# Kernel optimization log

Measured on AMD Instinct MI355X. Metric: run time of the kernel, lower is better.

The kernel has to match this reference:

```python
import jax, jax.numpy as jnp
import numpy as np

TILE = 16


def _tiled_hamilton_transform(tiles, weights):
    """tiles: [B, T, 16, 4]; weights: [T, 16, 16, 4] -> [B, T, 16, 4].

    Equivalent to broadcasting the Hamilton product to [B,T,16,16,4] and
    summing over dim=2, but expressed as 16 small einsum contractions so the
    large intermediate is never materialized.
    """
    a1, b1, c1, d1 = [tiles[..., k] for k in range(4)]      # each [B, T, 16]
    a2, b2, c2, d2 = [weights[..., k] for k in range(4)]    # each [T, 16, 16]

    def ctr(x, w):
        return jnp.einsum('bti,tij->btj', x, w)

    r_a = ctr(a1, a2) - ctr(b1, b2) - ctr(c1, c2) - ctr(d1, d2)
    r_b = ctr(a1, b2) + ctr(b1, a2) + ctr(c1, d2) - ctr(d1, c2)
    r_c = ctr(a1, c2) - ctr(b1, d2) + ctr(c1, a2) + ctr(d1, b2)
    r_d = ctr(a1, d2) + ctr(b1, c2) - ctr(c1, b2) + ctr(d1, a2)
    return jnp.stack([r_a, r_b, r_c, r_d], axis=-1)


def setup_inputs() -> dict:
    key = jax.random.key(0)
    k1, k2, k3 = jax.random.split(key, 3)
    x = jax.random.normal(k1, (65536, 256, 4), dtype=jnp.float32)
    phi_weights = jax.random.normal(k2, (16, 16, 16, 4), dtype=jnp.float32) * 0.02
    psi_weights = jax.random.normal(k3, (16, 16, 16, 4), dtype=jnp.float32) * 0.02
    return {"x": x, "phi_weights": phi_weights, "psi_weights": psi_weights}


def reference(x, phi_weights, psi_weights):
    B, D, _ = x.shape                      # D = manifold_dim = 256
    half_tiles = D // 2 // TILE            # = 8 = num_tiles // 2
    x1, x2 = jnp.split(x, 2, axis=1)       # each [B, 128, 4]
    x1_tiles = x1.reshape(B, half_tiles, TILE, 4)
    x2_tiles = x2.reshape(B, half_tiles, TILE, 4)

    f_out = _tiled_hamilton_transform(x2_tiles, phi_weights[:half_tiles])
    y1_tiles = x1_tiles + f_out
    g_out = _tiled_hamilton_transform(y1_tiles, psi_weights[half_tiles:])
    y2_tiles = x2_tiles + g_out

    y1 = y1_tiles.reshape(B, -1, 4)
    y2 = y2_tiles.reshape(B, -1, 4)
    return jnp.concatenate([y1, y2], axis=1)
```

## Files before the change

kernel.cpp:

```cpp
#include <hip/hip_runtime.h>
#include <hip/hip_bf16.h>


typedef __attribute__((ext_vector_type(8))) short bf16x8;
typedef __attribute__((ext_vector_type(4))) float f32x4;

static __device__ __forceinline__ unsigned short f2bf(float f) {
    unsigned u = __builtin_bit_cast(unsigned, f);
    unsigned r = 0x7FFFu + ((u >> 16) & 1u);
    return (unsigned short)((u + r) >> 16);
}

static __device__ __forceinline__ short hwbf(float f) {
    __hip_bfloat16 h = __float2bfloat16(f);
    return __builtin_bit_cast(short, h);
}

__global__ __launch_bounds__(256)
void prep_kernel(const float4* __restrict__ phi,
                 const float4* __restrict__ psi,
                 unsigned short* __restrict__ mt) {
    __shared__ float Phi[64][64];
    __shared__ float Psi[64][64];
    const int t   = blockIdx.x;
    const int tid = threadIdx.x;
    const int i   = tid >> 4, j = tid & 15;

    {
        float4 w = phi[t * 256 + i * 16 + j];
        float a = w.x, b = w.y, c = w.z, d = w.w;
        Phi[4*i+0][4*j+0]= a; Phi[4*i+0][4*j+1]= b; Phi[4*i+0][4*j+2]= c; Phi[4*i+0][4*j+3]= d;
        Phi[4*i+1][4*j+0]=-b; Phi[4*i+1][4*j+1]= a; Phi[4*i+1][4*j+2]=-d; Phi[4*i+1][4*j+3]= c;
        Phi[4*i+2][4*j+0]=-c; Phi[4*i+2][4*j+1]= d; Phi[4*i+2][4*j+2]= a; Phi[4*i+2][4*j+3]=-b;
        Phi[4*i+3][4*j+0]=-d; Phi[4*i+3][4*j+1]=-c; Phi[4*i+3][4*j+2]= b; Phi[4*i+3][4*j+3]= a;
        float4 v = psi[(8 + t) * 256 + i * 16 + j];
        a = v.x; b = v.y; c = v.z; d = v.w;
        Psi[4*i+0][4*j+0]= a; Psi[4*i+0][4*j+1]= b; Psi[4*i+0][4*j+2]= c; Psi[4*i+0][4*j+3]= d;
        Psi[4*i+1][4*j+0]=-b; Psi[4*i+1][4*j+1]= a; Psi[4*i+1][4*j+2]=-d; Psi[4*i+1][4*j+3]= c;
        Psi[4*i+2][4*j+0]=-c; Psi[4*i+2][4*j+1]= d; Psi[4*i+2][4*j+2]= a; Psi[4*i+2][4*j+3]=-b;
        Psi[4*i+3][4*j+0]=-d; Psi[4*i+3][4*j+1]=-c; Psi[4*i+3][4*j+2]= b; Psi[4*i+3][4*j+3]= a;
    }
    __syncthreads();

    unsigned short* m = mt + t * 16384;
    for (int e = tid; e < 16384; e += 256) {
        const int n = e >> 7, k = e & 127;
        if (n >= 64 && k >= 64) continue;
        float v;
        if (k < 64 && n < 64)       v = (k == n) ? 1.f : 0.f;
        else if (k >= 64)           v = Phi[k - 64][n];
        else                        v = Psi[k][n - 64];
        m[e] = f2bf(v);
    }
    const int r = tid & 63, c0 = (tid >> 6) * 16;
    float pk[16];
#pragma unroll
    for (int cc = 0; cc < 16; ++cc) pk[cc] = 0.f;
    for (int k = 0; k < 64; ++k) {
        const float fr = Phi[r][k];
#pragma unroll
        for (int cc = 0; cc < 16; ++cc) pk[cc] = fmaf(fr, Psi[k][c0 + cc], pk[cc]);
    }
#pragma unroll
    for (int cc = 0; cc < 16; ++cc) {
        const int c = c0 + cc;
        m[(64 + c) * 128 + (64 + r)] = f2bf(((r == c) ? 1.f : 0.f) + pk[cc]);
    }
}

__global__ __launch_bounds__(256)
void gemm_kernel(const float* __restrict__ x,
                 const unsigned short* __restrict__ mt,
                 float* __restrict__ out,
                 int ngroups) {
    const int tid  = threadIdx.x;
    const int lane = tid & 63, wid = tid >> 6;
    const int wm = wid >> 1, wn = wid & 1;
    const int ln = lane & 15, lk = lane >> 4;
    const int t  = blockIdx.x & 7;
    const int gs = gridDim.x >> 3;

    bf16x8 a[4][4];
    {
        const unsigned short* mtt = mt + t * 16384;
#pragma unroll
        for (int fn = 0; fn < 4; ++fn)
#pragma unroll
            for (int ks = 0; ks < 4; ++ks)
                a[fn][ks] = *(const bf16x8*)(mtt + (wn * 64 + fn * 16 + ln) * 128
                                                 + ks * 32 + lk * 8);
    }

    const int ca  = t * 64 + lk * 8;
    const int cob = (wn ? 512 : 0) + t * 64;

    float4 L[8];
    auto issue = [&](int gg) {
        const float* xr = x + ((size_t)gg * 32 + wm * 16 + ln) * 1024 + ca;
        L[0] = *(const float4*)(xr + 0);   L[1] = *(const float4*)(xr + 4);
        L[2] = *(const float4*)(xr + 32);  L[3] = *(const float4*)(xr + 36);
        L[4] = *(const float4*)(xr + 512); L[5] = *(const float4*)(xr + 516);
        L[6] = *(const float4*)(xr + 544); L[7] = *(const float4*)(xr + 548);
    };

    int g = blockIdx.x >> 3;
    if (g < ngroups) issue(g);

    while (g < ngroups) {
        bf16x8 bx[4];
#define PACK(kk, A, B) { \
        bx[kk][0] = hwbf(A.x); bx[kk][1] = hwbf(A.y); \
        bx[kk][2] = hwbf(A.z); bx[kk][3] = hwbf(A.w); \
        bx[kk][4] = hwbf(B.x); bx[kk][5] = hwbf(B.y); \
        bx[kk][6] = hwbf(B.z); bx[kk][7] = hwbf(B.w); }
        PACK(0, L[0], L[1]) PACK(1, L[2], L[3])
        PACK(2, L[4], L[5]) PACK(3, L[6], L[7])
#undef PACK

        const int gn = g + gs;
        if (gn < ngroups) issue(gn);

        f32x4 acc[4];
#pragma unroll
        for (int fn = 0; fn < 4; ++fn) acc[fn] = (f32x4)(0.f);
#pragma unroll
        for (int ks = 0; ks < 4; ++ks)
#pragma unroll
            for (int fn = 0; fn < 4; ++fn)
                acc[fn] = __builtin_amdgcn_mfma_f32_16x16x32_bf16(
                    a[fn][ks], bx[ks], acc[fn], 0, 0, 0);

        {
            float* orow = out + ((size_t)g * 32 + wm * 16 + ln) * 1024
                              + cob + lk * 4;
#pragma unroll
            for (int fn = 0; fn < 4; ++fn)
                __builtin_nontemporal_store(acc[fn], (f32x4*)(orow + fn * 16));
        }

        g = gn;
    }
}

extern "C" void kernel_launch(void* const* d_in, const int* in_sizes, int n_in,
                              void* d_out, int out_size, void* d_ws, size_t ws_size,
                              hipStream_t stream) {
    const float* x    = (const float*)d_in[0];
    const float4* phi = (const float4*)d_in[1];
    const float4* psi = (const float4*)d_in[2];
    unsigned short* mt = (unsigned short*)d_ws;
    float* out = (float*)d_out;

    const int rows    = in_sizes[0] / 1024;
    const int ngroups = rows / 32;
    const int blocks  = 8 * 96;

    prep_kernel<<<8, 256, 0, stream>>>(phi, psi, mt);
    gemm_kernel<<<blocks, 256, 0, stream>>>(x, mt, out, ngroups);
}
```

Baseline: 124.7 us.

## Split GEMM work across 4 N-waves with double-buffered 16-row loads

The GEMM kernel now assigns each of the four waves a 32-column slice of the output on a 16-row group, where before it used a 2x2 wave layout over a 32-row group. Input loads are double-buffered two groups ahead so more memory requests are in flight. The grid grows to 1024 blocks, and output stores switch from nontemporal to regular. This aims to hide more HBM latency in a memory-bound kernel, at the cost of each x row being loaded redundantly by all four waves and of more vector registers held by the extra buffer.

Result: slower. 197.7 us (+58.6%).

```diff
diff --git a/kernel.cpp b/kernel.cpp
--- a/kernel.cpp
+++ b/kernel.cpp
@@ -74,72 +74,66 @@
                  float* __restrict__ out,
                  int ngroups) {
     const int tid  = threadIdx.x;
-    const int lane = tid & 63, wid = tid >> 6;
-    const int wm = wid >> 1, wn = wid & 1;
+    const int lane = tid & 63;
+    const int wn   = tid >> 6;
     const int ln = lane & 15, lk = lane >> 4;
     const int t  = blockIdx.x & 7;
     const int gs = gridDim.x >> 3;
 
-    bf16x8 a[4][4];
+    bf16x8 a[2][4];
     {
         const unsigned short* mtt = mt + t * 16384;
 #pragma unroll
-        for (int fn = 0; fn < 4; ++fn)
+        for (int fn = 0; fn < 2; ++fn)
 #pragma unroll
             for (int ks = 0; ks < 4; ++ks)
-                a[fn][ks] = *(const bf16x8*)(mtt + (wn * 64 + fn * 16 + ln) * 128
+                a[fn][ks] = *(const bf16x8*)(mtt + (wn * 32 + fn * 16 + ln) * 128
                                                  + ks * 32 + lk * 8);
     }
 
     const int ca  = t * 64 + lk * 8;
-    const int cob = (wn ? 512 : 0) + t * 64;
+    const int cob = t * 64 + ((wn < 2) ? wn * 32 : 512 + (wn - 2) * 32);
 
-    float4 L[8];
-    auto issue = [&](int gg) {
-        const float* xr = x + ((size_t)gg * 32 + wm * 16 + ln) * 1024 + ca;
-        L[0] = *(const float4*)(xr + 0);   L[1] = *(const float4*)(xr + 4);
-        L[2] = *(const float4*)(xr + 32);  L[3] = *(const float4*)(xr + 36);
-        L[4] = *(const float4*)(xr + 512); L[5] = *(const float4*)(xr + 516);
-        L[6] = *(const float4*)(xr + 544); L[7] = *(const float4*)(xr + 548);
-    };
+    float4 LA[8], LB[8];
+#define ISSUE(Lbuf, gg) { \
+        const float* xr = x + ((size_t)(gg) * 16 + ln) * 1024 + ca; \
+        Lbuf[0] = *(const float4*)(xr + 0);   Lbuf[1] = *(const float4*)(xr + 4); \
+        Lbuf[2] = *(const float4*)(xr + 32);  Lbuf[3] = *(const float4*)(xr + 36); \
+        Lbuf[4] = *(const float4*)(xr + 512); Lbuf[5] = *(const float4*)(xr + 516); \
+        Lbuf[6] = *(const float4*)(xr + 544); Lbuf[7] = *(const float4*)(xr + 548); }
+
+#define PHASE(Lbuf, gg, gpre) { \
+        bf16x8 bx[4]; \
+        _Pragma("unroll") \
+        for (int kk = 0; kk < 4; ++kk) { \
+            bx[kk][0] = hwbf(Lbuf[2*kk].x);   bx[kk][1] = hwbf(Lbuf[2*kk].y); \
+            bx[kk][2] = hwbf(Lbuf[2*kk].z);   bx[kk][3] = hwbf(Lbuf[2*kk].w); \
+            bx[kk][4] = hwbf(Lbuf[2*kk+1].x); bx[kk][5] = hwbf(Lbuf[2*kk+1].y); \
+            bx[kk][6] = hwbf(Lbuf[2*kk+1].z); bx[kk][7] = hwbf(Lbuf[2*kk+1].w); \
+        } \
+        if ((gpre) < ngroups) ISSUE(Lbuf, gpre)           \
+        f32x4 acc[2]; \
+        acc[0] = (f32x4)(0.f); acc[1] = (f32x4)(0.f); \
+        _Pragma("unroll") \
+        for (int ks = 0; ks < 4; ++ks) { \
+            acc[0] = __builtin_amdgcn_mfma_f32_16x16x32_bf16(a[0][ks], bx[ks], acc[0], 0, 0, 0); \
+            acc[1] = __builtin_amdgcn_mfma_f32_16x16x32_bf16(a[1][ks], bx[ks], acc[1], 0, 0, 0); \
+        } \
+        float* orow = out + ((size_t)(gg) * 16 + ln) * 1024 + cob + lk * 4; \
+        *(f32x4*)(orow)      = acc[0]; \
+        *(f32x4*)(orow + 16) = acc[1]; }
 
     int g = blockIdx.x >> 3;
-    if (g < ngroups) issue(g);
+    if (g < ngroups)      ISSUE(LA, g)
+    if (g + gs < ngroups) ISSUE(LB, g + gs)
 
     while (g < ngroups) {
-        bf16x8 bx[4];
-#define PACK(kk, A, B) { \
-        bx[kk][0] = hwbf(A.x); bx[kk][1] = hwbf(A.y); \
-        bx[kk][2] = hwbf(A.z); bx[kk][3] = hwbf(A.w); \
-        bx[kk][4] = hwbf(B.x); bx[kk][5] = hwbf(B.y); \
-        bx[kk][6] = hwbf(B.z); bx[kk][7] = hwbf(B.w); }
-        PACK(0, L[0], L[1]) PACK(1, L[2], L[3])
-        PACK(2, L[4], L[5]) PACK(3, L[6], L[7])
-#undef PACK
-
-        const int gn = g + gs;
-        if (gn < ngroups) issue(gn);
-
-        f32x4 acc[4];
-#pragma unroll
-        for (int fn = 0; fn < 4; ++fn) acc[fn] = (f32x4)(0.f);
-#pragma unroll
-        for (int ks = 0; ks < 4; ++ks)
-#pragma unroll
-            for (int fn = 0; fn < 4; ++fn)
-                acc[fn] = __builtin_amdgcn_mfma_f32_16x16x32_bf16(
-                    a[fn][ks], bx[ks], acc[fn], 0, 0, 0);
-
-        {
-            float* orow = out + ((size_t)g * 32 + wm * 16 + ln) * 1024
-                              + cob + lk * 4;
-#pragma unroll
-            for (int fn = 0; fn < 4; ++fn)
-                __builtin_nontemporal_store(acc[fn], (f32x4*)(orow + fn * 16));
-        }
-
-        g = gn;
+        PHASE(LA, g, g + 2 * gs)
+        if (g + gs < ngroups) PHASE(LB, g + gs, g + 3 * gs)
+        g += 2 * gs;
     }
+#undef PHASE
+#undef ISSUE
 }
 
 extern "C" void kernel_launch(void* const* d_in, const int* in_sizes, int n_in,
@@ -152,8 +146,8 @@
     float* out = (float*)d_out;
 
     const int rows    = in_sizes[0] / 1024;
-    const int ngroups = rows / 32;
-    const int blocks  = 8 * 96;
+    const int ngroups = rows / 16;
+    const int blocks  = 8 * 128;
 
     prep_kernel<<<8, 256, 0, stream>>>(phi, psi, mt);
     gemm_kernel<<<blocks, 256, 0, stream>>>(x, mt, out, ngroups);
```

## Stage transform matrix in LDS and give each wave full N range

Applied to the files above, without the earlier changes.

The 128x128 bf16 transform matrix is now copied into shared memory once per block, and each wave reads A fragments from LDS inside the MFMA loop instead of holding half the matrix in registers. Each wave now covers all 128 output columns for 16 rows, so a block processes 64 rows per iteration and loads of x are no longer duplicated across the two wn waves. Nontemporal stores are replaced by plain stores, and the grid grows to 1024 blocks. The change removes redundant global reads of x but adds LDS traffic on every iteration and uses 32KB of shared memory per block, which may limit occupancy.

Measured after the change: 131.5 us. 1.05x slower.

```diff
diff --git a/kernel.cpp b/kernel.cpp
--- a/kernel.cpp
+++ b/kernel.cpp
@@ -73,73 +73,76 @@
                  const unsigned short* __restrict__ mt,
                  float* __restrict__ out,
                  int ngroups) {
+    __shared__ __align__(16) short Ms[128 * 128];
+
     const int tid  = threadIdx.x;
-    const int lane = tid & 63, wid = tid >> 6;
-    const int wm = wid >> 1, wn = wid & 1;
+    const int lane = tid & 63;
+    const int w    = tid >> 6;
     const int ln = lane & 15, lk = lane >> 4;
     const int t  = blockIdx.x & 7;
     const int gs = gridDim.x >> 3;
 
-    bf16x8 a[4][4];
     {
-        const unsigned short* mtt = mt + t * 16384;
+        const bf16x8* src = (const bf16x8*)(mt + t * 16384);
+        bf16x8* dst = (bf16x8*)Ms;
 #pragma unroll
-        for (int fn = 0; fn < 4; ++fn)
-#pragma unroll
-            for (int ks = 0; ks < 4; ++ks)
-                a[fn][ks] = *(const bf16x8*)(mtt + (wn * 64 + fn * 16 + ln) * 128
-                                                 + ks * 32 + lk * 8);
+        for (int i = 0; i < 8; ++i) dst[tid + i * 256] = src[tid + i * 256];
     }
+    __syncthreads();
 
-    const int ca  = t * 64 + lk * 8;
-    const int cob = (wn ? 512 : 0) + t * 64;
+    const int ca = t * 64 + lk * 8;
 
     float4 L[8];
-    auto issue = [&](int gg) {
-        const float* xr = x + ((size_t)gg * 32 + wm * 16 + ln) * 1024 + ca;
-        L[0] = *(const float4*)(xr + 0);   L[1] = *(const float4*)(xr + 4);
-        L[2] = *(const float4*)(xr + 32);  L[3] = *(const float4*)(xr + 36);
-        L[4] = *(const float4*)(xr + 512); L[5] = *(const float4*)(xr + 516);
-        L[6] = *(const float4*)(xr + 544); L[7] = *(const float4*)(xr + 548);
-    };
+#define ISSUE(gg) { \
+        const float* xr = x + ((size_t)(gg) * 64 + w * 16 + ln) * 1024 + ca; \
+        L[0] = *(const float4*)(xr + 0);   L[1] = *(const float4*)(xr + 4); \
+        L[2] = *(const float4*)(xr + 32);  L[3] = *(const float4*)(xr + 36); \
+        L[4] = *(const float4*)(xr + 512); L[5] = *(const float4*)(xr + 516); \
+        L[6] = *(const float4*)(xr + 544); L[7] = *(const float4*)(xr + 548); }
 
     int g = blockIdx.x >> 3;
-    if (g < ngroups) issue(g);
+    if (g < ngroups) ISSUE(g)
 
     while (g < ngroups) {
         bf16x8 bx[4];
-#define PACK(kk, A, B) { \
-        bx[kk][0] = hwbf(A.x); bx[kk][1] = hwbf(A.y); \
-        bx[kk][2] = hwbf(A.z); bx[kk][3] = hwbf(A.w); \
-        bx[kk][4] = hwbf(B.x); bx[kk][5] = hwbf(B.y); \
-        bx[kk][6] = hwbf(B.z); bx[kk][7] = hwbf(B.w); }
-        PACK(0, L[0], L[1]) PACK(1, L[2], L[3])
-        PACK(2, L[4], L[5]) PACK(3, L[6], L[7])
-#undef PACK
+#pragma unroll
+        for (int kk = 0; kk < 4; ++kk) {
+            bx[kk][0] = hwbf(L[2*kk].x);   bx[kk][1] = hwbf(L[2*kk].y);
+            bx[kk][2] = hwbf(L[2*kk].z);   bx[kk][3] = hwbf(L[2*kk].w);
+            bx[kk][4] = hwbf(L[2*kk+1].x); bx[kk][5] = hwbf(L[2*kk+1].y);
+            bx[kk][6] = hwbf(L[2*kk+1].z); bx[kk][7] = hwbf(L[2*kk+1].w);
+        }
 
         const int gn = g + gs;
-        if (gn < ngroups) issue(gn);
+        if (gn < ngroups) ISSUE(gn)
 
-        f32x4 acc[4];
+        f32x4 acc[8];
 #pragma unroll
-        for (int fn = 0; fn < 4; ++fn) acc[fn] = (f32x4)(0.f);
+        for (int fn = 0; fn < 8; ++fn) acc[fn] = (f32x4)(0.f);
 #pragma unroll
-        for (int ks = 0; ks < 4; ++ks)
+        for (int ks = 0; ks < 4; ++ks) {
 #pragma unroll
-            for (int fn = 0; fn < 4; ++fn)
+            for (int fn = 0; fn < 8; ++fn) {
+                const bf16x8 af = *(const bf16x8*)(Ms + (fn * 16 + ln) * 128
+                                                      + ks * 32 + lk * 8);
                 acc[fn] = __builtin_amdgcn_mfma_f32_16x16x32_bf16(
-                    a[fn][ks], bx[ks], acc[fn], 0, 0, 0);
+                    af, bx[ks], acc[fn], 0, 0, 0);
+            }
+        }
 
         {
-            float* orow = out + ((size_t)g * 32 + wm * 16 + ln) * 1024
-                              + cob + lk * 4;
+            float* orow = out + ((size_t)g * 64 + w * 16 + ln) * 1024;
 #pragma unroll
-            for (int fn = 0; fn < 4; ++fn)
-                __builtin_nontemporal_store(acc[fn], (f32x4*)(orow + fn * 16));
+            for (int fn = 0; fn < 8; ++fn) {
+                const int col = ((fn < 4) ? t * 64 + fn * 16
+                                          : 512 + t * 64 + (fn - 4) * 16) + lk * 4;
+                *(f32x4*)(orow + col) = acc[fn];
+            }
         }
 
         g = gn;
     }
+#undef ISSUE
 }
 
 extern "C" void kernel_launch(void* const* d_in, const int* in_sizes, int n_in,
@@ -152,8 +155,8 @@
     float* out = (float*)d_out;
 
     const int rows    = in_sizes[0] / 1024;
-    const int ngroups = rows / 32;
-    const int blocks  = 8 * 96;
+    const int ngroups = rows / 64;
+    const int blocks  = 8 * 128;
 
     prep_kernel<<<8, 256, 0, stream>>>(phi, psi, mt);
     gemm_kernel<<<blocks, 256, 0, stream>>>(x, mt, out, ngroups);
```
